# Kernel tuning notes

Hardware: AMD Instinct MI355X
Metric: run time of the kernel (lower is better)

The kernel has to match this reference:

```python
import jax, jax.numpy as jnp
import numpy as np

N, D, H, C, E, K = 32768, 1024, 512, 512, 8, 2

def setup_inputs() -> dict:
    key = jax.random.key(0)
    ks = jax.random.split(key, 7)
    s = lambda fan_in: 1.0 / np.sqrt(fan_in)
    return {
        "x":  jax.random.normal(ks[0], (N, D), dtype=jnp.float32),
        "W1": jax.random.uniform(ks[1], (E, D, H), minval=-s(D), maxval=s(D), dtype=jnp.float32),
        "b1": jax.random.uniform(ks[2], (E, H), minval=-s(D), maxval=s(D), dtype=jnp.float32),
        "W2": jax.random.uniform(ks[3], (E, H, C), minval=-s(H), maxval=s(H), dtype=jnp.float32),
        "b2": jax.random.uniform(ks[4], (E, C), minval=-s(H), maxval=s(H), dtype=jnp.float32),
        "Wg": jax.random.uniform(ks[5], (D, E), minval=-s(D), maxval=s(D), dtype=jnp.float32),
        "bg": jax.random.uniform(ks[6], (E,), minval=-s(D), maxval=s(D), dtype=jnp.float32),
    }

def reference(x, W1, b1, W2, b2, Wg, bg):
    # Gating: dense gate vector with softmax(top-k logits) scattered into top-k slots
    gate_logits = x @ Wg + bg                               # [N, E]
    top_vals, top_idx = jax.lax.top_k(gate_logits, K)       # [N, K]
    gate = jnp.zeros_like(gate_logits).at[
        jnp.arange(x.shape[0])[:, None], top_idx
    ].set(jax.nn.softmax(top_vals, axis=-1))                # [N, E]
    # Dense all-experts FFN (as in the original module; dropout inactive at eval)
    h = jax.nn.relu(jnp.einsum('nd,edh->enh', x, W1) + b1[:, None, :])   # [E, N, H]
    out = jnp.einsum('enh,ehc->enc', h, W2) + b2[:, None, :]             # [E, N, C]
    # Masked weighted combine
    return jnp.einsum('ne,enc->nc', gate, out)              # [N, C]
```

## Files before the change

kernel.cpp:

```cpp
#include <hip/hip_runtime.h>

#define NTOK 32768
#define DDIM 1024
#define HDIM 512
#define CDIM 512
#define NEXP 8

#define BM 128
#define BN 128
#define BK 64
#define MAXTILE 520

typedef __attribute__((ext_vector_type(8))) __bf16 bf16x8;
typedef __attribute__((ext_vector_type(4))) float f32x4;
typedef __attribute__((ext_vector_type(4))) unsigned short us4;
typedef __attribute__((ext_vector_type(8))) unsigned short us8;

static __device__ __forceinline__ unsigned short f2bf(float f) {
  union { float f; unsigned u; } v; v.f = f;
  unsigned u = v.u;
  u += 0x7FFFu + ((u >> 16) & 1u);
  return (unsigned short)(u >> 16);
}

static __device__ __forceinline__ float bf2f(unsigned short s) {
  union { unsigned u; float f; } v;
  v.u = ((unsigned)s) << 16;
  return v.f;
}

static __device__ __forceinline__ void gl_lds16(const void* g, void* l) {
  __builtin_amdgcn_global_load_lds(
      (const __attribute__((address_space(1))) unsigned int*)(unsigned long long)g,
      (__attribute__((address_space(3))) unsigned int*)(unsigned)(unsigned long long)l,
      16, 0, 0);
}

static __device__ __forceinline__ void fence_dma_then_barrier() {
  __builtin_amdgcn_sched_barrier(0);
  asm volatile("s_waitcnt vmcnt(0)" ::: "memory");
  __builtin_amdgcn_sched_barrier(0);
  __syncthreads();
}

static __device__ __forceinline__ void fence_lds_then_barrier() {
  __builtin_amdgcn_sched_barrier(0);
  asm volatile("s_waitcnt lgkmcnt(0)" ::: "memory");
  __builtin_amdgcn_sched_barrier(0);
  __syncthreads();
}

__global__ __launch_bounds__(256) void transpose_bf16_kernel(
    const float* __restrict__ in, unsigned short* __restrict__ out,
    int R, int Cc) {
  __shared__ float tile[32][33];
  int e = blockIdx.z;
  int c0 = blockIdx.x * 32, r0 = blockIdx.y * 32;
  const float* src = in + (size_t)e * R * Cc;
  unsigned short* dst = out + (size_t)e * R * Cc;
  int tx = threadIdx.x, ty = threadIdx.y;
#pragma unroll
  for (int i = 0; i < 32; i += 8)
    tile[ty + i][tx] = src[(size_t)(r0 + ty + i) * Cc + (c0 + tx)];
  __syncthreads();
#pragma unroll
  for (int i = 0; i < 32; i += 8)
    dst[(size_t)(c0 + ty + i) * R + (r0 + tx)] = f2bf(tile[tx][ty + i]);
}

#define GWPITCH 1064
#define XSLOT 1056

__global__ __launch_bounds__(256) void gate_kernel(
    const float* __restrict__ x, const float* __restrict__ Wg,
    const float* __restrict__ bg, int* __restrict__ sel,
    float* __restrict__ wpair, unsigned short* __restrict__ xb) {
  __shared__ float wg_lds[NEXP * GWPITCH];
  __shared__ float xs[4][XSLOT];

  int t = threadIdx.x;
  for (int i = t; i < DDIM * NEXP / 4; i += 256) {
    f32x4 v = *(const f32x4*)(Wg + (size_t)i * 4);
    int d = i >> 1;
    int e0 = (i & 1) * 4;
    int dsk = d + 4 * (d >> 7);
#pragma unroll
    for (int z = 0; z < 4; ++z)
      wg_lds[(e0 + z) * GWPITCH + dsk] = v[z];
  }
  __syncthreads();

  int wave = t >> 6, lane = t & 63;
  int g = lane >> 3, e = lane & 7;
  float* xslab = xs[wave];
  const float* wgrow = wg_lds + e * GWPITCH + g * 132;
  const float* xsg = xslab + g * 132;
  double bge = (double)bg[e];

  int n0 = blockIdx.x * 32 + wave * 8;
  f32x4 ld[4], ldn[4];
  {
    const f32x4* xrow = (const f32x4*)(x + (size_t)n0 * DDIM);
#pragma unroll
    for (int j = 0; j < 4; ++j) ld[j] = xrow[j * 64 + lane];
  }

#pragma unroll 1
  for (int r = 0; r < 8; ++r) {
    int n = n0 + r;
    unsigned short* xbr = xb + (size_t)n * DDIM;
#pragma unroll
    for (int j = 0; j < 4; ++j) {
      int d0 = j * 256 + lane * 4;
      *(f32x4*)&xslab[d0 + 4 * (d0 >> 7)] = ld[j];
      us4 o;
#pragma unroll
      for (int z = 0; z < 4; ++z) o[z] = f2bf(ld[j][z]);
      *(us4*)&xbr[d0] = o;
    }
    if (r < 7) {
      const f32x4* xr2 = (const f32x4*)(x + (size_t)(n + 1) * DDIM);
#pragma unroll
      for (int j = 0; j < 4; ++j) ldn[j] = xr2[j * 64 + lane];
    }
    float s0 = 0.0f, c0 = 0.0f, s1 = 0.0f, c1 = 0.0f;
#pragma unroll
    for (int k = 0; k < 32; ++k) {
      f32x4 xv = *(const f32x4*)&xsg[4 * k];
      f32x4 wv = *(const f32x4*)&wgrow[4 * k];
#pragma unroll
      for (int z = 0; z < 4; z += 2) {
        float p0 = xv[z] * wv[z];
        float y0 = p0 - c0;
        float t0 = s0 + y0;
        c0 = (t0 - s0) - y0;
        s0 = t0;
        float p1 = xv[z + 1] * wv[z + 1];
        float y1 = p1 - c1;
        float t1 = s1 + y1;
        c1 = (t1 - s1) - y1;
        s1 = t1;
      }
    }
    double p = ((double)s0 + (double)c0) + ((double)s1 + (double)c1);
    p += __shfl_xor(p, 8, 64);
    p += __shfl_xor(p, 16, 64);
    p += __shfl_xor(p, 32, 64);
    double mylg = p + bge;
    double lg[NEXP];
#pragma unroll
    for (int ee = 0; ee < NEXP; ++ee) lg[ee] = __shfl(mylg, ee, 64);
    if (lane == 0) {
      int e0i = 0;
#pragma unroll
      for (int ee = 1; ee < NEXP; ++ee) if (lg[ee] > lg[e0i]) e0i = ee;
      int e1i = (e0i == 0) ? 1 : 0;
#pragma unroll
      for (int ee = 0; ee < NEXP; ++ee)
        if (ee != e0i && lg[ee] > lg[e1i]) e1i = ee;
      float w1 = 1.0f / (1.0f + expf((float)(lg[e0i] - lg[e1i])));
      float w0 = 1.0f - w1;
      sel[n] = e0i | (e1i << 4);
      wpair[n * 2] = w0;
      wpair[n * 2 + 1] = w1;
    }
#pragma unroll
    for (int j = 0; j < 4; ++j) ld[j] = ldn[j];
  }
}

__global__ __launch_bounds__(1024) void build_lists_kernel(
    const int* __restrict__ sel, int* __restrict__ counts,
    int* __restrict__ lists) {
  int e = blockIdx.x;
  int t = threadIdx.x;
  __shared__ int sc[1024];
  int base = t * (NTOK / 1024);
  int cnt = 0;
#pragma unroll
  for (int i = 0; i < NTOK / 1024; ++i) {
    int s = sel[base + i];
    cnt += ((s & 15) == e) || (((s >> 4) & 15) == e);
  }
  sc[t] = cnt;
  __syncthreads();
  for (int d = 1; d < 1024; d <<= 1) {
    int v = (t >= d) ? sc[t - d] : 0;
    __syncthreads();
    sc[t] += v;
    __syncthreads();
  }
  int off = sc[t] - cnt;
#pragma unroll
  for (int i = 0; i < NTOK / 1024; ++i) {
    int s = sel[base + i];
    if ((s & 15) == e)
      lists[e * NTOK + off++] = (base + i) * 2;
    else if (((s >> 4) & 15) == e)
      lists[e * NTOK + off++] = (base + i) * 2 + 1;
  }
  if (t == 1023) counts[e] = sc[1023];
}

__global__ __launch_bounds__(256) void make_tiles_kernel(
    const int* __restrict__ counts, int* __restrict__ tiles) {
  __shared__ int off[NEXP + 1];
  int t = threadIdx.x;
  if (t == 0) {
    int s = 0;
    for (int e = 0; e < NEXP; ++e) { off[e] = s; s += (counts[e] + BM - 1) / BM; }
    off[NEXP] = s;
    tiles[0] = s;
  }
  __syncthreads();
  for (int e = 0; e < NEXP; ++e) {
    int base = off[e], cnt = off[e + 1] - off[e];
    for (int k = t; k < cnt; k += 256) {
      tiles[1 + 2 * (base + k)] = e;
      tiles[2 + 2 * (base + k)] = k * BM;
    }
  }
}

static __device__ __forceinline__ bool decode_tile(
    const int* tiles, const int* counts, int& e, int& ne, int& row0, int& col0) {
  int i = blockIdx.x;
  int xcd = i & 7, slot = i >> 3;
  int col = slot & 3, tslot = slot >> 2;
  int rt = tslot * 8 + xcd;
  if (rt >= tiles[0]) return false;
  e = tiles[1 + 2 * rt];
  row0 = tiles[2 + 2 * rt];
  ne = counts[e];
  col0 = col * BN;
  return true;
}

__global__ __launch_bounds__(256) void gemm1_kernel(
    const unsigned short* __restrict__ xb, const unsigned short* __restrict__ W1t,
    const float* __restrict__ b1, const int* __restrict__ lists,
    const int* __restrict__ counts, const int* __restrict__ tiles,
    unsigned short* __restrict__ h) {
  int e, ne, row0, col0;
  if (!decode_tile(tiles, counts, e, ne, row0, col0)) return;

  __shared__ __attribute__((aligned(128))) unsigned short sA[BM * BK];
  __shared__ __attribute__((aligned(128))) unsigned short sB[BN * BK];
  __shared__ int sTok[BM];

  int t = threadIdx.x;
  if (t < BM) {
    int r = row0 + t;
    sTok[t] = (r < ne) ? lists[e * NTOK + r] : -1;
  }
  __syncthreads();

  int srow = t >> 3;
  int sslot = (t & 7) ^ (srow & 7);
  const unsigned short* aSrc[4];
  const unsigned short* bSrc[4];
  unsigned short* aDst[4];
  unsigned short* bDst[4];
  int wbase = (t >> 6) * 512;
#pragma unroll
  for (int j = 0; j < 4; ++j) {
    int p = sTok[j * 32 + srow];
    int tok = (p < 0) ? 0 : (p >> 1);
    aSrc[j] = xb + (size_t)tok * DDIM + sslot * 8;
    int c = col0 + j * 32 + srow;
    bSrc[j] = W1t + ((size_t)e * HDIM + c) * DDIM + sslot * 8;
    aDst[j] = &sA[j * 2048 + wbase];
    bDst[j] = &sB[j * 2048 + wbase];
  }

  int wave = t >> 6, lane = t & 63;
  int wr = wave >> 1, wc = wave & 1;
  int fr = lane & 15, fg = lane >> 4;

  f32x4 acc[4][4];
#pragma unroll
  for (int m = 0; m < 4; ++m)
#pragma unroll
    for (int nn = 0; nn < 4; ++nn) acc[m][nn] = (f32x4)0.0f;

  const int NKT = DDIM / BK;
  for (int kt = 0; kt < NKT; ++kt) {
#pragma unroll
    for (int j = 0; j < 4; ++j) {
      gl_lds16(aSrc[j] + kt * BK, aDst[j]);
      gl_lds16(bSrc[j] + kt * BK, bDst[j]);
    }
    fence_dma_then_barrier();
#pragma unroll
    for (int ks = 0; ks < 2; ++ks) {
      int sl = (fg + ks * 4) ^ (fr & 7);
      bf16x8 af[4], bfr[4];
#pragma unroll
      for (int m = 0; m < 4; ++m)
        af[m] = *(const bf16x8*)&sA[(wr * 64 + m * 16 + fr) * 64 + sl * 8];
#pragma unroll
      for (int nn = 0; nn < 4; ++nn)
        bfr[nn] = *(const bf16x8*)&sB[(wc * 64 + nn * 16 + fr) * 64 + sl * 8];
#pragma unroll
      for (int m = 0; m < 4; ++m)
#pragma unroll
        for (int nn = 0; nn < 4; ++nn)
          acc[m][nn] = __builtin_amdgcn_mfma_f32_16x16x32_bf16(
              af[m], bfr[nn], acc[m][nn], 0, 0, 0);
    }
    fence_lds_then_barrier();
  }

  int cBase = col0 + wc * 64 + fr;
  float b1c[4];
#pragma unroll
  for (int nn = 0; nn < 4; ++nn) b1c[nn] = b1[e * HDIM + cBase + nn * 16];
#pragma unroll
  for (int m = 0; m < 4; ++m) {
#pragma unroll
    for (int q = 0; q < 4; ++q) {
      int rloc = wr * 64 + m * 16 + fg * 4 + q;
      if (row0 + rloc < ne) {
        int p = sTok[rloc];
        unsigned short* hr = h + (size_t)p * HDIM;
#pragma unroll
        for (int nn = 0; nn < 4; ++nn) {
          float v = acc[m][nn][q] + b1c[nn];
          v = fmaxf(v, 0.0f);
          hr[cBase + nn * 16] = f2bf(v);
        }
      }
    }
  }
}

__global__ __launch_bounds__(256) void gemm2_kernel(
    const unsigned short* __restrict__ h, const unsigned short* __restrict__ W2t,
    const float* __restrict__ b2, const int* __restrict__ lists,
    const int* __restrict__ counts, const int* __restrict__ tiles,
    unsigned short* __restrict__ obuf) {
  int e, ne, row0, col0;
  if (!decode_tile(tiles, counts, e, ne, row0, col0)) return;

  __shared__ __attribute__((aligned(128))) unsigned short sA[BM * BK];
  __shared__ __attribute__((aligned(128))) unsigned short sB[BN * BK];
  __shared__ int sTok[BM];

  int t = threadIdx.x;
  if (t < BM) {
    int r = row0 + t;
    sTok[t] = (r < ne) ? lists[e * NTOK + r] : -1;
  }
  __syncthreads();

  int srow = t >> 3;
  int sslot = (t & 7) ^ (srow & 7);
  const unsigned short* aSrc[4];
  const unsigned short* bSrc[4];
  unsigned short* aDst[4];
  unsigned short* bDst[4];
  int wbase = (t >> 6) * 512;
#pragma unroll
  for (int j = 0; j < 4; ++j) {
    int p = sTok[j * 32 + srow];
    int pp = (p < 0) ? 0 : p;
    aSrc[j] = h + (size_t)pp * HDIM + sslot * 8;
    int c = col0 + j * 32 + srow;
    bSrc[j] = W2t + ((size_t)e * CDIM + c) * HDIM + sslot * 8;
    aDst[j] = &sA[j * 2048 + wbase];
    bDst[j] = &sB[j * 2048 + wbase];
  }

  int wave = t >> 6, lane = t & 63;
  int wr = wave >> 1, wc = wave & 1;
  int fr = lane & 15, fg = lane >> 4;

  f32x4 acc[4][4];
#pragma unroll
  for (int m = 0; m < 4; ++m)
#pragma unroll
    for (int nn = 0; nn < 4; ++nn) acc[m][nn] = (f32x4)0.0f;

  const int NKT = HDIM / BK;
  for (int kt = 0; kt < NKT; ++kt) {
#pragma unroll
    for (int j = 0; j < 4; ++j) {
      gl_lds16(aSrc[j] + kt * BK, aDst[j]);
      gl_lds16(bSrc[j] + kt * BK, bDst[j]);
    }
    fence_dma_then_barrier();
#pragma unroll
    for (int ks = 0; ks < 2; ++ks) {
      int sl = (fg + ks * 4) ^ (fr & 7);
      bf16x8 af[4], bfr[4];
#pragma unroll
      for (int m = 0; m < 4; ++m)
        af[m] = *(const bf16x8*)&sA[(wr * 64 + m * 16 + fr) * 64 + sl * 8];
#pragma unroll
      for (int nn = 0; nn < 4; ++nn)
        bfr[nn] = *(const bf16x8*)&sB[(wc * 64 + nn * 16 + fr) * 64 + sl * 8];
#pragma unroll
      for (int m = 0; m < 4; ++m)
#pragma unroll
        for (int nn = 0; nn < 4; ++nn)
          acc[m][nn] = __builtin_amdgcn_mfma_f32_16x16x32_bf16(
              af[m], bfr[nn], acc[m][nn], 0, 0, 0);
    }
    fence_lds_then_barrier();
  }

  int cBase = col0 + wc * 64 + fr;
  float b2c[4];
#pragma unroll
  for (int nn = 0; nn < 4; ++nn) b2c[nn] = b2[e * CDIM + cBase + nn * 16];
#pragma unroll
  for (int m = 0; m < 4; ++m) {
#pragma unroll
    for (int q = 0; q < 4; ++q) {
      int rloc = wr * 64 + m * 16 + fg * 4 + q;
      if (row0 + rloc < ne) {
        int p = sTok[rloc];
        unsigned short* orow = obuf + (size_t)p * CDIM;
#pragma unroll
        for (int nn = 0; nn < 4; ++nn)
          orow[cBase + nn * 16] = f2bf(acc[m][nn][q] + b2c[nn]);
      }
    }
  }
}

__global__ __launch_bounds__(256) void combine_kernel(
    const float* __restrict__ wpair, float* __restrict__ out) {
  const unsigned short* obuf = (const unsigned short*)out;
  int t = threadIdx.x;
  int n = blockIdx.x * 4 + (t >> 6);
  int c = (t & 63) * 8;
  us8 a = *(const us8*)&obuf[(size_t)(2 * n) * CDIM + c];
  us8 b = *(const us8*)&obuf[(size_t)(2 * n + 1) * CDIM + c];
  float w0 = wpair[2 * n], w1 = wpair[2 * n + 1];
  f32x4 r0, r1;
#pragma unroll
  for (int z = 0; z < 4; ++z) {
    r0[z] = w0 * bf2f(a[z]) + w1 * bf2f(b[z]);
    r1[z] = w0 * bf2f(a[z + 4]) + w1 * bf2f(b[z + 4]);
  }
  __syncthreads();
  *(f32x4*)&out[(size_t)n * CDIM + c] = r0;
  *(f32x4*)&out[(size_t)n * CDIM + c + 4] = r1;
}

extern "C" void kernel_launch(void* const* d_in, const int* in_sizes, int n_in,
                              void* d_out, int out_size, void* d_ws, size_t ws_size,
                              hipStream_t stream) {
  const float* x  = (const float*)d_in[0];
  const float* W1 = (const float*)d_in[1];
  const float* b1 = (const float*)d_in[2];
  const float* W2 = (const float*)d_in[3];
  const float* b2 = (const float*)d_in[4];
  const float* Wg = (const float*)d_in[5];
  const float* bg = (const float*)d_in[6];
  float* out = (float*)d_out;
  char* ws = (char*)d_ws;

  int* counts = (int*)ws;
  float* wpair = (float*)(ws + 256);
  int* sel = (int*)(ws + 256 + 262144);
  int* lists = (int*)(ws + 256 + 262144 + 131072);
  int* tiles = (int*)(ws + 256 + 262144 + 131072 + 1048576);
  unsigned short* W1t = (unsigned short*)(ws + 256 + 262144 + 131072 + 1048576 + 8192);
  unsigned short* W2t = W1t + (size_t)NEXP * HDIM * DDIM;
  unsigned short* hbuf = W2t + (size_t)NEXP * CDIM * HDIM;

  unsigned short* xb = (unsigned short*)d_out;
  unsigned short* obuf = (unsigned short*)d_out;

  hipLaunchKernelGGL(transpose_bf16_kernel, dim3(HDIM / 32, DDIM / 32, NEXP),
                     dim3(32, 8), 0, stream, W1, W1t, DDIM, HDIM);
  hipLaunchKernelGGL(transpose_bf16_kernel, dim3(CDIM / 32, HDIM / 32, NEXP),
                     dim3(32, 8), 0, stream, W2, W2t, HDIM, CDIM);
  hipLaunchKernelGGL(gate_kernel, dim3(NTOK / 32), dim3(256), 0, stream,
                     x, Wg, bg, sel, wpair, xb);
  hipLaunchKernelGGL(build_lists_kernel, dim3(NEXP), dim3(1024), 0, stream,
                     sel, counts, lists);
  hipLaunchKernelGGL(make_tiles_kernel, dim3(1), dim3(256), 0, stream,
                     counts, tiles);
  hipLaunchKernelGGL(gemm1_kernel, dim3((MAXTILE / 8) * 4 * 8), dim3(256),
                     0, stream, xb, W1t, b1, lists, counts, tiles, hbuf);
  hipLaunchKernelGGL(gemm2_kernel, dim3((MAXTILE / 8) * 4 * 8), dim3(256),
                     0, stream, hbuf, W2t, b2, lists, counts, tiles, obuf);
  hipLaunchKernelGGL(combine_kernel, dim3(NTOK / 4), dim3(256), 0, stream,
                     wpair, out);
}
```

Baseline: 248.5 us.

## Double-buffer LDS in both expert GEMMs to overlap global loads with MFMA

Both grouped GEMM kernels now keep two LDS buffers for the A and B tiles. The next K-tile is issued with global_load_lds into the alternate buffer before the current tile is consumed, and the wait becomes vmcnt(8) so only the older batch must land. This is meant to hide global-memory latency behind MFMA work instead of stalling on every K-step. It doubles LDS use to about 64KB per block, which may reduce occupancy.

```diff
diff --git a/kernel.cpp b/kernel.cpp
--- a/kernel.cpp
+++ b/kernel.cpp
@@ -34,20 +34,6 @@
       (const __attribute__((address_space(1))) unsigned int*)(unsigned long long)g,
       (__attribute__((address_space(3))) unsigned int*)(unsigned)(unsigned long long)l,
       16, 0, 0);
-}
-
-static __device__ __forceinline__ void fence_dma_then_barrier() {
-  __builtin_amdgcn_sched_barrier(0);
-  asm volatile("s_waitcnt vmcnt(0)" ::: "memory");
-  __builtin_amdgcn_sched_barrier(0);
-  __syncthreads();
-}
-
-static __device__ __forceinline__ void fence_lds_then_barrier() {
-  __builtin_amdgcn_sched_barrier(0);
-  asm volatile("s_waitcnt lgkmcnt(0)" ::: "memory");
-  __builtin_amdgcn_sched_barrier(0);
-  __syncthreads();
 }
 
 __global__ __launch_bounds__(256) void transpose_bf16_kernel(
@@ -244,8 +230,8 @@
   int e, ne, row0, col0;
   if (!decode_tile(tiles, counts, e, ne, row0, col0)) return;
 
-  __shared__ __attribute__((aligned(128))) unsigned short sA[BM * BK];
-  __shared__ __attribute__((aligned(128))) unsigned short sB[BN * BK];
+  __shared__ __attribute__((aligned(128))) unsigned short sA[2][BM * BK];
+  __shared__ __attribute__((aligned(128))) unsigned short sB[2][BN * BK];
   __shared__ int sTok[BM];
 
   int t = threadIdx.x;
@@ -259,8 +245,7 @@
   int sslot = (t & 7) ^ (srow & 7);
   const unsigned short* aSrc[4];
   const unsigned short* bSrc[4];
-  unsigned short* aDst[4];
-  unsigned short* bDst[4];
+  int dOff[4];
   int wbase = (t >> 6) * 512;
 #pragma unroll
   for (int j = 0; j < 4; ++j) {
@@ -269,8 +254,7 @@
     aSrc[j] = xb + (size_t)tok * DDIM + sslot * 8;
     int c = col0 + j * 32 + srow;
     bSrc[j] = W1t + ((size_t)e * HDIM + c) * DDIM + sslot * 8;
-    aDst[j] = &sA[j * 2048 + wbase];
-    bDst[j] = &sB[j * 2048 + wbase];
+    dOff[j] = j * 2048 + wbase;
   }
 
   int wave = t >> 6, lane = t & 63;
@@ -284,23 +268,38 @@
     for (int nn = 0; nn < 4; ++nn) acc[m][nn] = (f32x4)0.0f;
 
   const int NKT = DDIM / BK;
+#pragma unroll
+  for (int j = 0; j < 4; ++j) {
+    gl_lds16(aSrc[j], &sA[0][dOff[j]]);
+    gl_lds16(bSrc[j], &sB[0][dOff[j]]);
+  }
   for (int kt = 0; kt < NKT; ++kt) {
-#pragma unroll
-    for (int j = 0; j < 4; ++j) {
-      gl_lds16(aSrc[j] + kt * BK, aDst[j]);
-      gl_lds16(bSrc[j] + kt * BK, bDst[j]);
-    }
-    fence_dma_then_barrier();
+    int cur = kt & 1;
+    if (kt + 1 < NKT) {
+#pragma unroll
+      for (int j = 0; j < 4; ++j) {
+        gl_lds16(aSrc[j] + (kt + 1) * BK, &sA[cur ^ 1][dOff[j]]);
+        gl_lds16(bSrc[j] + (kt + 1) * BK, &sB[cur ^ 1][dOff[j]]);
+      }
+      __builtin_amdgcn_sched_barrier(0);
+      asm volatile("s_waitcnt vmcnt(8)" ::: "memory");
+    } else {
+      __builtin_amdgcn_sched_barrier(0);
+      asm volatile("s_waitcnt vmcnt(0)" ::: "memory");
+    }
+    __builtin_amdgcn_sched_barrier(0);
+    __builtin_amdgcn_s_barrier();
+    __builtin_amdgcn_sched_barrier(0);
 #pragma unroll
     for (int ks = 0; ks < 2; ++ks) {
       int sl = (fg + ks * 4) ^ (fr & 7);
       bf16x8 af[4], bfr[4];
 #pragma unroll
       for (int m = 0; m < 4; ++m)
-        af[m] = *(const bf16x8*)&sA[(wr * 64 + m * 16 + fr) * 64 + sl * 8];
+        af[m] = *(const bf16x8*)&sA[cur][(wr * 64 + m * 16 + fr) * 64 + sl * 8];
 #pragma unroll
       for (int nn = 0; nn < 4; ++nn)
-        bfr[nn] = *(const bf16x8*)&sB[(wc * 64 + nn * 16 + fr) * 64 + sl * 8];
+        bfr[nn] = *(const bf16x8*)&sB[cur][(wc * 64 + nn * 16 + fr) * 64 + sl * 8];
 #pragma unroll
       for (int m = 0; m < 4; ++m)
 #pragma unroll
@@ -308,7 +307,10 @@
           acc[m][nn] = __builtin_amdgcn_mfma_f32_16x16x32_bf16(
               af[m], bfr[nn], acc[m][nn], 0, 0, 0);
     }
-    fence_lds_then_barrier();
+    __builtin_amdgcn_sched_barrier(0);
+    asm volatile("s_waitcnt lgkmcnt(0)" ::: "memory");
+    __builtin_amdgcn_sched_barrier(0);
+    __builtin_amdgcn_s_barrier();
   }
 
   int cBase = col0 + wc * 64 + fr;
@@ -342,8 +344,8 @@
   int e, ne, row0, col0;
   if (!decode_tile(tiles, counts, e, ne, row0, col0)) return;
 
-  __shared__ __attribute__((aligned(128))) unsigned short sA[BM * BK];
-  __shared__ __attribute__((aligned(128))) unsigned short sB[BN * BK];
+  __shared__ __attribute__((aligned(128))) unsigned short sA[2][BM * BK];
+  __shared__ __attribute__((aligned(128))) unsigned short sB[2][BN * BK];
   __shared__ int sTok[BM];
 
   int t = threadIdx.x;
@@ -357,8 +359,7 @@
   int sslot = (t & 7) ^ (srow & 7);
   const unsigned short* aSrc[4];
   const unsigned short* bSrc[4];
-  unsigned short* aDst[4];
-  unsigned short* bDst[4];
+  int dOff[4];
   int wbase = (t >> 6) * 512;
 #pragma unroll
   for (int j = 0; j < 4; ++j) {
@@ -367,8 +368,7 @@
     aSrc[j] = h + (size_t)pp * HDIM + sslot * 8;
     int c = col0 + j * 32 + srow;
     bSrc[j] = W2t + ((size_t)e * CDIM + c) * HDIM + sslot * 8;
-    aDst[j] = &sA[j * 2048 + wbase];
-    bDst[j] = &sB[j * 2048 + wbase];
+    dOff[j] = j * 2048 + wbase;
   }
 
   int wave = t >> 6, lane = t & 63;
@@ -382,23 +382,38 @@
     for (int nn = 0; nn < 4; ++nn) acc[m][nn] = (f32x4)0.0f;
 
   const int NKT = HDIM / BK;
+#pragma unroll
+  for (int j = 0; j < 4; ++j) {
+    gl_lds16(aSrc[j], &sA[0][dOff[j]]);
+    gl_lds16(bSrc[j], &sB[0][dOff[j]]);
+  }
   for (int kt = 0; kt < NKT; ++kt) {
-#pragma unroll
-    for (int j = 0; j < 4; ++j) {
-      gl_lds16(aSrc[j] + kt * BK, aDst[j]);
-      gl_lds16(bSrc[j] + kt * BK, bDst[j]);
-    }
-    fence_dma_then_barrier();
+    int cur = kt & 1;
+    if (kt + 1 < NKT) {
+#pragma unroll
+      for (int j = 0; j < 4; ++j) {
+        gl_lds16(aSrc[j] + (kt + 1) * BK, &sA[cur ^ 1][dOff[j]]);
+        gl_lds16(bSrc[j] + (kt + 1) * BK, &sB[cur ^ 1][dOff[j]]);
+      }
+      __builtin_amdgcn_sched_barrier(0);
+      asm volatile("s_waitcnt vmcnt(8)" ::: "memory");
+    } else {
+      __builtin_amdgcn_sched_barrier(0);
+      asm volatile("s_waitcnt vmcnt(0)" ::: "memory");
+    }
+    __builtin_amdgcn_sched_barrier(0);
+    __builtin_amdgcn_s_barrier();
+    __builtin_amdgcn_sched_barrier(0);
 #pragma unroll
     for (int ks = 0; ks < 2; ++ks) {
       int sl = (fg + ks * 4) ^ (fr & 7);
       bf16x8 af[4], bfr[4];
 #pragma unroll
       for (int m = 0; m < 4; ++m)
-        af[m] = *(const bf16x8*)&sA[(wr * 64 + m * 16 + fr) * 64 + sl * 8];
+        af[m] = *(const bf16x8*)&sA[cur][(wr * 64 + m * 16 + fr) * 64 + sl * 8];
 #pragma unroll
       for (int nn = 0; nn < 4; ++nn)
-        bfr[nn] = *(const bf16x8*)&sB[(wc * 64 + nn * 16 + fr) * 64 + sl * 8];
+        bfr[nn] = *(const bf16x8*)&sB[cur][(wc * 64 + nn * 16 + fr) * 64 + sl * 8];
 #pragma unroll
       for (int m = 0; m < 4; ++m)
 #pragma unroll
@@ -406,7 +421,10 @@
           acc[m][nn] = __builtin_amdgcn_mfma_f32_16x16x32_bf16(
               af[m], bfr[nn], acc[m][nn], 0, 0, 0);
     }
-    fence_lds_then_barrier();
+    __builtin_amdgcn_sched_barrier(0);
+    asm volatile("s_waitcnt lgkmcnt(0)" ::: "memory");
+    __builtin_amdgcn_sched_barrier(0);
+    __builtin_amdgcn_s_barrier();
   }
 
   int cBase = col0 + wc * 64 + fr;
```

Measured after the change: 276.3 us. 1.11x slower.

## Double-buffer LDS tiles with BK=32 to overlap global loads and MFMA

Applied to the files above, without the earlier changes.

Both grouped GEMM kernels now use two LDS buffers with a K-step of 32 instead of a single buffer with K-step 64. The next tile's global-to-LDS DMA is issued before computing on the current buffer, with one fence per step instead of two. This is meant to hide global load latency behind MFMA work, and it changes the swizzle pattern to match the 32-wide rows. In exchange it doubles the number of K iterations and barriers, and LDS use per block stays the same.

```diff
diff --git a/kernel.cpp b/kernel.cpp
--- a/kernel.cpp
+++ b/kernel.cpp
@@ -8,7 +8,7 @@
 
 #define BM 128
 #define BN 128
-#define BK 64
+#define BKS 32
 #define MAXTILE 520
 
 typedef __attribute__((ext_vector_type(8))) __bf16 bf16x8;
@@ -43,11 +43,12 @@
   __syncthreads();
 }
 
-static __device__ __forceinline__ void fence_lds_then_barrier() {
+static __device__ __forceinline__ void pipe_fence() {
   __builtin_amdgcn_sched_barrier(0);
-  asm volatile("s_waitcnt lgkmcnt(0)" ::: "memory");
+  asm volatile("s_waitcnt vmcnt(0)" ::: "memory");
   __builtin_amdgcn_sched_barrier(0);
-  __syncthreads();
+  __builtin_amdgcn_s_barrier();
+  __builtin_amdgcn_sched_barrier(0);
 }
 
 __global__ __launch_bounds__(256) void transpose_bf16_kernel(
@@ -244,8 +245,8 @@
   int e, ne, row0, col0;
   if (!decode_tile(tiles, counts, e, ne, row0, col0)) return;
 
-  __shared__ __attribute__((aligned(128))) unsigned short sA[BM * BK];
-  __shared__ __attribute__((aligned(128))) unsigned short sB[BN * BK];
+  __shared__ __attribute__((aligned(128))) unsigned short sA[2][BM * BKS];
+  __shared__ __attribute__((aligned(128))) unsigned short sB[2][BN * BKS];
   __shared__ int sTok[BM];
 
   int t = threadIdx.x;
@@ -255,27 +256,26 @@
   }
   __syncthreads();
 
-  int srow = t >> 3;
-  int sslot = (t & 7) ^ (srow & 7);
-  const unsigned short* aSrc[4];
-  const unsigned short* bSrc[4];
-  unsigned short* aDst[4];
-  unsigned short* bDst[4];
+  int srow = t >> 2;
+  int lslot = (t & 3) ^ ((t >> 3) & 3);
+  const unsigned short* aSrc[2];
+  const unsigned short* bSrc[2];
+  int dOff[2];
   int wbase = (t >> 6) * 512;
 #pragma unroll
-  for (int j = 0; j < 4; ++j) {
-    int p = sTok[j * 32 + srow];
+  for (int j = 0; j < 2; ++j) {
+    int p = sTok[j * 64 + srow];
     int tok = (p < 0) ? 0 : (p >> 1);
-    aSrc[j] = xb + (size_t)tok * DDIM + sslot * 8;
-    int c = col0 + j * 32 + srow;
-    bSrc[j] = W1t + ((size_t)e * HDIM + c) * DDIM + sslot * 8;
-    aDst[j] = &sA[j * 2048 + wbase];
-    bDst[j] = &sB[j * 2048 + wbase];
+    aSrc[j] = xb + (size_t)tok * DDIM + lslot * 8;
+    int c = col0 + j * 64 + srow;
+    bSrc[j] = W1t + ((size_t)e * HDIM + c) * DDIM + lslot * 8;
+    dOff[j] = j * 2048 + wbase;
   }
 
   int wave = t >> 6, lane = t & 63;
   int wr = wave >> 1, wc = wave & 1;
   int fr = lane & 15, fg = lane >> 4;
+  int sl = (fg ^ ((fr >> 1) & 3)) * 8;
 
   f32x4 acc[4][4];
 #pragma unroll
@@ -283,33 +283,46 @@
 #pragma unroll
     for (int nn = 0; nn < 4; ++nn) acc[m][nn] = (f32x4)0.0f;
 
-  const int NKT = DDIM / BK;
-  for (int kt = 0; kt < NKT; ++kt) {
-#pragma unroll
-    for (int j = 0; j < 4; ++j) {
-      gl_lds16(aSrc[j] + kt * BK, aDst[j]);
-      gl_lds16(bSrc[j] + kt * BK, bDst[j]);
-    }
-    fence_dma_then_barrier();
-#pragma unroll
-    for (int ks = 0; ks < 2; ++ks) {
-      int sl = (fg + ks * 4) ^ (fr & 7);
-      bf16x8 af[4], bfr[4];
-#pragma unroll
-      for (int m = 0; m < 4; ++m)
-        af[m] = *(const bf16x8*)&sA[(wr * 64 + m * 16 + fr) * 64 + sl * 8];
-#pragma unroll
-      for (int nn = 0; nn < 4; ++nn)
-        bfr[nn] = *(const bf16x8*)&sB[(wc * 64 + nn * 16 + fr) * 64 + sl * 8];
-#pragma unroll
-      for (int m = 0; m < 4; ++m)
-#pragma unroll
-        for (int nn = 0; nn < 4; ++nn)
-          acc[m][nn] = __builtin_amdgcn_mfma_f32_16x16x32_bf16(
-              af[m], bfr[nn], acc[m][nn], 0, 0, 0);
-    }
-    fence_lds_then_barrier();
-  }
+#define G1_STAGE(buf, kt)                                         \
+  {                                                               \
+    _Pragma("unroll")                                             \
+    for (int j = 0; j < 2; ++j) {                                 \
+      gl_lds16(aSrc[j] + (kt) * BKS, &sA[buf][dOff[j]]);          \
+      gl_lds16(bSrc[j] + (kt) * BKS, &sB[buf][dOff[j]]);          \
+    }                                                             \
+  }
+
+#define G1_COMPUTE(buf)                                           \
+  {                                                               \
+    bf16x8 af[4], bfr[4];                                         \
+    _Pragma("unroll")                                             \
+    for (int m = 0; m < 4; ++m)                                   \
+      af[m] = *(const bf16x8*)&sA[buf][(wr * 64 + m * 16 + fr) * BKS + sl]; \
+    _Pragma("unroll")                                             \
+    for (int nn = 0; nn < 4; ++nn)                                \
+      bfr[nn] = *(const bf16x8*)&sB[buf][(wc * 64 + nn * 16 + fr) * BKS + sl]; \
+    _Pragma("unroll")                                             \
+    for (int m = 0; m < 4; ++m)                                   \
+      _Pragma("unroll")                                           \
+      for (int nn = 0; nn < 4; ++nn)                              \
+        acc[m][nn] = __builtin_amdgcn_mfma_f32_16x16x32_bf16(     \
+            af[m], bfr[nn], acc[m][nn], 0, 0, 0);                 \
+  }
+
+  const int NKT = DDIM / BKS;
+  G1_STAGE(0, 0);
+  fence_dma_then_barrier();
+#pragma unroll 1
+  for (int kt = 0; kt < NKT; kt += 2) {
+    G1_STAGE(1, kt + 1);
+    G1_COMPUTE(0);
+    pipe_fence();
+    if (kt + 2 < NKT) G1_STAGE(0, kt + 2);
+    G1_COMPUTE(1);
+    pipe_fence();
+  }
+#undef G1_STAGE
+#undef G1_COMPUTE
 
   int cBase = col0 + wc * 64 + fr;
   float b1c[4];
@@ -342,8 +355,8 @@
   int e, ne, row0, col0;
   if (!decode_tile(tiles, counts, e, ne, row0, col0)) return;
 
-  __shared__ __attribute__((aligned(128))) unsigned short sA[BM * BK];
-  __shared__ __attribute__((aligned(128))) unsigned short sB[BN * BK];
+  __shared__ __attribute__((aligned(128))) unsigned short sA[2][BM * BKS];
+  __shared__ __attribute__((aligned(128))) unsigned short sB[2][BN * BKS];
   __shared__ int sTok[BM];
 
   int t = threadIdx.x;
@@ -353,27 +366,26 @@
   }
   __syncthreads();
 
-  int srow = t >> 3;
-  int sslot = (t & 7) ^ (srow & 7);
-  const unsigned short* aSrc[4];
-  const unsigned short* bSrc[4];
-  unsigned short* aDst[4];
-  unsigned short* bDst[4];
+  int srow = t >> 2;
+  int lslot = (t & 3) ^ ((t >> 3) & 3);
+  const unsigned short* aSrc[2];
+  const unsigned short* bSrc[2];
+  int dOff[2];
   int wbase = (t >> 6) * 512;
 #pragma unroll
-  for (int j = 0; j < 4; ++j) {
-    int p = sTok[j * 32 + srow];
+  for (int j = 0; j < 2; ++j) {
+    int p = sTok[j * 64 + srow];
     int pp = (p < 0) ? 0 : p;
-    aSrc[j] = h + (size_t)pp * HDIM + sslot * 8;
-    int c = col0 + j * 32 + srow;
-    bSrc[j] = W2t + ((size_t)e * CDIM + c) * HDIM + sslot * 8;
-    aDst[j] = &sA[j * 2048 + wbase];
-    bDst[j] = &sB[j * 2048 + wbase];
+    aSrc[j] = h + (size_t)pp * HDIM + lslot * 8;
+    int c = col0 + j * 64 + srow;
+    bSrc[j] = W2t + ((size_t)e * CDIM + c) * HDIM + lslot * 8;
+    dOff[j] = j * 2048 + wbase;
   }
 
   int wave = t >> 6, lane = t & 63;
   int wr = wave >> 1, wc = wave & 1;
   int fr = lane & 15, fg = lane >> 4;
+  int sl = (fg ^ ((fr >> 1) & 3)) * 8;
 
   f32x4 acc[4][4];
 #pragma unroll
@@ -381,33 +393,46 @@
 #pragma unroll
     for (int nn = 0; nn < 4; ++nn) acc[m][nn] = (f32x4)0.0f;
 
-  const int NKT = HDIM / BK;
-  for (int kt = 0; kt < NKT; ++kt) {
-#pragma unroll
-    for (int j = 0; j < 4; ++j) {
-      gl_lds16(aSrc[j] + kt * BK, aDst[j]);
-      gl_lds16(bSrc[j] + kt * BK, bDst[j]);
-    }
-    fence_dma_then_barrier();
-#pragma unroll
-    for (int ks = 0; ks < 2; ++ks) {
-      int sl = (fg + ks * 4) ^ (fr & 7);
-      bf16x8 af[4], bfr[4];
-#pragma unroll
-      for (int m = 0; m < 4; ++m)
-        af[m] = *(const bf16x8*)&sA[(wr * 64 + m * 16 + fr) * 64 + sl * 8];
-#pragma unroll
-      for (int nn = 0; nn < 4; ++nn)
-        bfr[nn] = *(const bf16x8*)&sB[(wc * 64 + nn * 16 + fr) * 64 + sl * 8];
-#pragma unroll
-      for (int m = 0; m < 4; ++m)
-#pragma unroll
-        for (int nn = 0; nn < 4; ++nn)
-          acc[m][nn] = __builtin_amdgcn_mfma_f32_16x16x32_bf16(
-              af[m], bfr[nn], acc[m][nn], 0, 0, 0);
-    }
-    fence_lds_then_barrier();
-  }
+#define G2_STAGE(buf, kt)                                         \
+  {                                                               \
+    _Pragma("unroll")                                             \
+    for (int j = 0; j < 2; ++j) {                                 \
+      gl_lds16(aSrc[j] + (kt) * BKS, &sA[buf][dOff[j]]);          \
+      gl_lds16(bSrc[j] + (kt) * BKS, &sB[buf][dOff[j]]);          \
+    }                                                             \
+  }
+
+#define G2_COMPUTE(buf)                                           \
+  {                                                               \
+    bf16x8 af[4], bfr[4];                                         \
+    _Pragma("unroll")                                             \
+    for (int m = 0; m < 4; ++m)                                   \
+      af[m] = *(const bf16x8*)&sA[buf][(wr * 64 + m * 16 + fr) * BKS + sl]; \
+    _Pragma("unroll")                                             \
+    for (int nn = 0; nn < 4; ++nn)                                \
+      bfr[nn] = *(const bf16x8*)&sB[buf][(wc * 64 + nn * 16 + fr) * BKS + sl]; \
+    _Pragma("unroll")                                             \
+    for (int m = 0; m < 4; ++m)                                   \
+      _Pragma("unroll")                                           \
+      for (int nn = 0; nn < 4; ++nn)                              \
+        acc[m][nn] = __builtin_amdgcn_mfma_f32_16x16x32_bf16(     \
+            af[m], bfr[nn], acc[m][nn], 0, 0, 0);                 \
+  }
+
+  const int NKT = HDIM / BKS;
+  G2_STAGE(0, 0);
+  fence_dma_then_barrier();
+#pragma unroll 1
+  for (int kt = 0; kt < NKT; kt += 2) {
+    G2_STAGE(1, kt + 1);
+    G2_COMPUTE(0);
+    pipe_fence();
+    if (kt + 2 < NKT) G2_STAGE(0, kt + 2);
+    G2_COMPUTE(1);
+    pipe_fence();
+  }
+#undef G2_STAGE
+#undef G2_COMPUTE
 
   int cBase = col0 + wc * 64 + fr;
   float b2c[4];
```

Result: slower. 304.7 us (+22.7%).
